# Kernel tuning notes

Measured on AMD Instinct MI355X. Metric: run time of the kernel, lower is better.

Reference implementation:

```python
import jax, jax.numpy as jnp
import numpy as np

DIM = 1024
SEQ = 4096
HEADS = 16
DH = 64
KPROJ = 64
MLP = 4096
EPS = 1e-5


def layer_norm(x, g, b):
    mu = jnp.mean(x, axis=-1, keepdims=True)
    var = jnp.mean(jnp.square(x - mu), axis=-1, keepdims=True)
    return (x - mu) * jax.lax.rsqrt(var + EPS) * g + b


def setup_inputs() -> dict:
    key = jax.random.key(0)
    ks = jax.random.split(key, 12)
    s = 0.02
    return {
        "x": jax.random.normal(ks[0], (4, SEQ, DIM), jnp.float32),
        "Wq": jax.random.normal(ks[1], (DIM, HEADS * DH), jnp.float32) * s,
        "Wk": jax.random.normal(ks[2], (DIM, HEADS * DH), jnp.float32) * s,
        "Wv": jax.random.normal(ks[3], (DIM, HEADS * DH), jnp.float32) * s,
        "E": jax.random.normal(ks[4], (SEQ, KPROJ), jnp.float32),
        "Fm": jax.random.normal(ks[5], (SEQ, KPROJ), jnp.float32),
        "Wo": jax.random.normal(ks[6], (HEADS * DH, DIM), jnp.float32) * s,
        "bo": jnp.zeros((DIM,), jnp.float32),
        "ln1_g": jnp.ones((DIM,), jnp.float32),
        "ln1_b": jnp.zeros((DIM,), jnp.float32),
        "ln2_g": jnp.ones((DIM,), jnp.float32),
        "ln2_b": jnp.zeros((DIM,), jnp.float32),
        "W1": jax.random.normal(ks[7], (DIM, MLP), jnp.float32) * s,
        "b1": jnp.zeros((MLP,), jnp.float32),
        "W2": jax.random.normal(ks[8], (MLP, DIM), jnp.float32) * s,
        "b2": jnp.zeros((DIM,), jnp.float32),
    }


def reference(x, Wq, Wk, Wv, E, Fm, Wo, bo, ln1_g, ln1_b, ln2_g, ln2_b, W1, b1, W2, b2):
    B, S, D = x.shape
    scale = DH ** -0.5
    # --- Linformer attention (pre-norm) ---
    xn = layer_norm(x, ln1_g, ln1_b)
    q = (xn @ Wq).reshape(B, S, HEADS, DH).transpose(0, 2, 1, 3)  # b h s d
    k = (xn @ Wk).reshape(B, S, HEADS, DH).transpose(0, 2, 1, 3)
    v = (xn @ Wv).reshape(B, S, HEADS, DH).transpose(0, 2, 1, 3)
    # Faithful to source: i and n are summed independently (rank-1 projection)
    kE = jnp.einsum('bhid,nk->bhkd', k, E)   # b h k d
    vF = jnp.einsum('bhid,nk->bhkd', v, Fm)  # b h k d
    dots = jnp.einsum('bhsd,bhkd->bhsk', q, kE) * scale
    attn = jax.nn.softmax(dots, axis=-1)
    out = jnp.einsum('bhsk,bhkd->bhsd', attn, vF)
    out = out.transpose(0, 2, 1, 3).reshape(B, S, HEADS * DH)
    x = x + out @ Wo + bo
    # --- MLP (pre-norm) ---
    xn2 = layer_norm(x, ln2_g, ln2_b)
    h = jax.nn.gelu(xn2 @ W1 + b1, approximate=False)
    x = x + h @ W2 + b2
    return x
```

## Files before the change

kernel.cpp:

```cpp
#include <hip/hip_runtime.h>
#include <hip/hip_bf16.h>

#define DIMD 1024
#define SEQL 4096
#define BATCH 4
#define NHEADS 16
#define DHEAD 64
#define KPROJ 64
#define MLPD 4096
#define NTOK (BATCH*SEQL)
#define EPSV 1e-5f
#define TPB 4

using short8 = __attribute__((ext_vector_type(8))) short;
using f32x4  = __attribute__((ext_vector_type(4))) float;

__device__ __forceinline__ float wave_reduce_sum(float v) {
    #pragma unroll
    for (int off = 32; off > 0; off >>= 1) v += __shfl_down(v, off, 64);
    return v;
}

__device__ __forceinline__ void async_cp16(const unsigned short* g, unsigned short* l) {
    __builtin_amdgcn_global_load_lds(
        (const __attribute__((address_space(1))) unsigned int*)g,
        (__attribute__((address_space(3))) unsigned int*)l,
        16, 0, 0);
}

__global__ __launch_bounds__(256) void k_stats1(const float* __restrict__ x,
                                                float* __restrict__ stats) {
    int t = blockIdx.x;
    const float4 x4 = *(const float4*)(x + (size_t)t*DIMD + threadIdx.x*4);
    float s  = x4.x + x4.y + x4.z + x4.w;
    float ss = x4.x*x4.x + x4.y*x4.y + x4.z*x4.z + x4.w*x4.w;
    s = wave_reduce_sum(s); ss = wave_reduce_sum(ss);
    __shared__ float rs[4], rss[4];
    int wave = threadIdx.x >> 6, lane = threadIdx.x & 63;
    if (lane == 0) { rs[wave] = s; rss[wave] = ss; }
    __syncthreads();
    if (threadIdx.x == 0) {
        float S1 = rs[0]+rs[1]+rs[2]+rs[3];
        float S2 = rss[0]+rss[1]+rss[2]+rss[3];
        float mu = S1 * (1.0f/DIMD);
        float var = S2 * (1.0f/DIMD) - mu*mu;
        stats[2*t]   = mu;
        stats[2*t+1] = rsqrtf(var + EPSV);
    }
}

__global__ __launch_bounds__(256) void k_xnsum(const float* __restrict__ x,
                                               const float* __restrict__ stats,
                                               const float* __restrict__ g1,
                                               const float* __restrict__ be1,
                                               float* __restrict__ xnsum) {
    int b = blockIdx.x >> 7, sc = blockIdx.x & 127;
    int d = threadIdx.x * 4;
    int t0 = b*SEQL + sc*32;
    float a0=0,a1=0,a2=0,a3=0;
    for (int s = 0; s < 32; s++) {
        int t = t0 + s;
        float mu = stats[2*t], rstd = stats[2*t+1];
        const float4 x4 = *(const float4*)(x + (size_t)t*DIMD + d);
        a0 += (x4.x-mu)*rstd; a1 += (x4.y-mu)*rstd;
        a2 += (x4.z-mu)*rstd; a3 += (x4.w-mu)*rstd;
    }
    const float4 g4 = *(const float4*)(g1 + d);
    const float4 b4 = *(const float4*)(be1 + d);
    atomicAdd(&xnsum[b*DIMD + d + 0], a0*g4.x + 32.0f*b4.x);
    atomicAdd(&xnsum[b*DIMD + d + 1], a1*g4.y + 32.0f*b4.y);
    atomicAdd(&xnsum[b*DIMD + d + 2], a2*g4.z + 32.0f*b4.z);
    atomicAdd(&xnsum[b*DIMD + d + 3], a3*g4.w + 32.0f*b4.w);
}

__global__ __launch_bounds__(256) void k_efsum(const float* __restrict__ E,
                                               const float* __restrict__ Fm,
                                               float* __restrict__ Esum,
                                               float* __restrict__ Fsum) {
    int g = blockIdx.x;
    int k = threadIdx.x & 63, seg = threadIdx.x >> 6;
    __shared__ float red[4][64];
    int n0 = g*256 + seg*64;
    float pe = 0, pf = 0;
    for (int i = 0; i < 64; i++) {
        pe += E [(size_t)(n0+i)*KPROJ + k];
        pf += Fm[(size_t)(n0+i)*KPROJ + k];
    }
    red[seg][k] = pe; __syncthreads();
    if (seg == 0) atomicAdd(&Esum[k], red[0][k]+red[1][k]+red[2][k]+red[3][k]);
    __syncthreads();
    red[seg][k] = pf; __syncthreads();
    if (seg == 0) atomicAdd(&Fsum[k], red[0][k]+red[1][k]+red[2][k]+red[3][k]);
}

__global__ __launch_bounds__(256) void k_kvsum(const float* __restrict__ xnsum,
                                               const float* __restrict__ Wk,
                                               const float* __restrict__ Wv,
                                               float* __restrict__ Ksum,
                                               float* __restrict__ Vsum) {
    int i = blockIdx.x;
    int dc = i & 3, jc = (i >> 2) & 3, which = (i >> 4) & 1, b = i >> 5;
    const float* W = which ? Wv : Wk;
    float* outp = which ? Vsum : Ksum;
    int j = jc*256 + threadIdx.x;
    __shared__ float xs[256];
    xs[threadIdx.x] = xnsum[b*DIMD + dc*256 + threadIdx.x];
    __syncthreads();
    float acc = 0;
    #pragma unroll 8
    for (int dd = 0; dd < 256; dd++)
        acc += xs[dd] * W[(size_t)(dc*256 + dd)*DIMD + j];
    atomicAdd(&outp[b*DIMD + j], acc);
}

__global__ __launch_bounds__(256) void k_mt(const float* __restrict__ Wq,
                                            const float* __restrict__ Ksum,
                                            float* __restrict__ Mt) {
    int i = blockIdx.x;
    int dc = i & 3, h = (i >> 2) & 15, b = i >> 6;
    __shared__ float ks[DHEAD];
    if (threadIdx.x < DHEAD) ks[threadIdx.x] = Ksum[b*DIMD + h*DHEAD + threadIdx.x];
    __syncthreads();
    int d = dc*256 + threadIdx.x;
    float acc = 0;
    #pragma unroll 8
    for (int j = 0; j < DHEAD; j++) acc += Wq[(size_t)d*DIMD + h*DHEAD + j] * ks[j];
    Mt[((size_t)b*NHEADS + h)*DIMD + d] = acc;
}

__global__ __launch_bounds__(256) void k_p(const float* __restrict__ Wo,
                                           const float* __restrict__ Vsum,
                                           float* __restrict__ P) {
    int i = blockIdx.x;
    int dc = i & 3, h = (i >> 2) & 15, b = i >> 6;
    __shared__ float vs[DHEAD];
    if (threadIdx.x < DHEAD) vs[threadIdx.x] = Vsum[b*DIMD + h*DHEAD + threadIdx.x];
    __syncthreads();
    int d = dc*256 + threadIdx.x;
    float acc = 0;
    #pragma unroll 8
    for (int j = 0; j < DHEAD; j++) acc += vs[j] * Wo[(size_t)(h*DHEAD + j)*DIMD + d];
    P[((size_t)b*NHEADS + h)*DIMD + d] = acc;
}

__global__ __launch_bounds__(256) void k_attn_apply(
    const float* __restrict__ x, const float* __restrict__ stats,
    const float* __restrict__ Mt, const float* __restrict__ P,
    const float* __restrict__ Esum, const float* __restrict__ Fsum,
    const float* __restrict__ g1, const float* __restrict__ be1,
    const float* __restrict__ bo,
    const float* __restrict__ g2, const float* __restrict__ be2,
    float* __restrict__ y, __hip_bfloat16* __restrict__ xn2) {
    __shared__ float red[TPB][NHEADS][4];
    __shared__ float w_s[TPB][NHEADS];
    __shared__ float red2[TPB][8];
    __shared__ float st2[TPB][2];
    const int t0 = blockIdx.x * TPB;
    const int b = t0 >> 12;
    const int tid = threadIdx.x;
    const int wave = tid >> 6, lane = tid & 63;
    const int d4 = tid * 4;

    const float4 g14 = *(const float4*)(g1 + d4);
    const float4 b14 = *(const float4*)(be1 + d4);
    float4 xf[TPB], xn[TPB];
    #pragma unroll
    for (int t = 0; t < TPB; t++) {
        xf[t] = *(const float4*)(x + (size_t)(t0+t)*DIMD + d4);
        float mu = stats[2*(t0+t)], rstd = stats[2*(t0+t)+1];
        xn[t].x = (xf[t].x-mu)*rstd*g14.x + b14.x;
        xn[t].y = (xf[t].y-mu)*rstd*g14.y + b14.y;
        xn[t].z = (xf[t].z-mu)*rstd*g14.z + b14.z;
        xn[t].w = (xf[t].w-mu)*rstd*g14.w + b14.w;
    }
    #pragma unroll
    for (int h = 0; h < NHEADS; h++) {
        const float4 m4 = *(const float4*)(Mt + ((size_t)b*NHEADS + h)*DIMD + d4);
        #pragma unroll
        for (int t = 0; t < TPB; t++) {
            float p = xn[t].x*m4.x + xn[t].y*m4.y + xn[t].z*m4.z + xn[t].w*m4.w;
            p = wave_reduce_sum(p);
            if (lane == 0) red[t][h][wave] = p;
        }
    }
    __syncthreads();
    {
        const float scale = 0.125f;
        const float ek = Esum[lane], fk = Fsum[lane];
        for (int pi = wave; pi < TPB*NHEADS; pi += 4) {
            int t = pi >> 4, h = pi & 15;
            float qk = red[t][h][0]+red[t][h][1]+red[t][h][2]+red[t][h][3];
            float logit = qk * scale * ek;
            float m = logit;
            #pragma unroll
            for (int off = 32; off > 0; off >>= 1) m = fmaxf(m, __shfl_down(m, off, 64));
            m = __shfl(m, 0, 64);
            float e = expf(logit - m);
            float s1 = e, s2 = e * fk;
            #pragma unroll
            for (int off = 32; off > 0; off >>= 1) {
                s1 += __shfl_down(s1, off, 64);
                s2 += __shfl_down(s2, off, 64);
            }
            if (lane == 0) w_s[t][h] = s2 / s1;
        }
    }
    __syncthreads();
    const float4 bo4 = *(const float4*)(bo + d4);
    #pragma unroll
    for (int t = 0; t < TPB; t++) {
        xf[t].x += bo4.x; xf[t].y += bo4.y; xf[t].z += bo4.z; xf[t].w += bo4.w;
    }
    #pragma unroll
    for (int h = 0; h < NHEADS; h++) {
        const float4 p4 = *(const float4*)(P + ((size_t)b*NHEADS + h)*DIMD + d4);
        #pragma unroll
        for (int t = 0; t < TPB; t++) {
            float wv = w_s[t][h];
            xf[t].x += wv*p4.x; xf[t].y += wv*p4.y;
            xf[t].z += wv*p4.z; xf[t].w += wv*p4.w;
        }
    }
    #pragma unroll
    for (int t = 0; t < TPB; t++) {
        *(float4*)(y + (size_t)(t0+t)*DIMD + d4) = xf[t];
        float s  = xf[t].x+xf[t].y+xf[t].z+xf[t].w;
        float ss = xf[t].x*xf[t].x+xf[t].y*xf[t].y+xf[t].z*xf[t].z+xf[t].w*xf[t].w;
        s = wave_reduce_sum(s); ss = wave_reduce_sum(ss);
        if (lane == 0) { red2[t][wave] = s; red2[t][4+wave] = ss; }
    }
    __syncthreads();
    if (tid < TPB) {
        float S1 = red2[tid][0]+red2[tid][1]+red2[tid][2]+red2[tid][3];
        float S2 = red2[tid][4]+red2[tid][5]+red2[tid][6]+red2[tid][7];
        float m2 = S1*(1.0f/DIMD);
        float v2 = S2*(1.0f/DIMD) - m2*m2;
        st2[tid][0] = m2; st2[tid][1] = rsqrtf(v2 + EPSV);
    }
    __syncthreads();
    const float4 g24 = *(const float4*)(g2 + d4);
    const float4 b24 = *(const float4*)(be2 + d4);
    #pragma unroll
    for (int t = 0; t < TPB; t++) {
        float mu2 = st2[t][0], rs2 = st2[t][1];
        union { __hip_bfloat16 h4[4]; uint2 v; } pk;
        pk.h4[0] = __float2bfloat16((xf[t].x-mu2)*rs2*g24.x + b24.x);
        pk.h4[1] = __float2bfloat16((xf[t].y-mu2)*rs2*g24.y + b24.y);
        pk.h4[2] = __float2bfloat16((xf[t].z-mu2)*rs2*g24.z + b24.z);
        pk.h4[3] = __float2bfloat16((xf[t].w-mu2)*rs2*g24.w + b24.w);
        *(uint2*)((char*)(xn2 + (size_t)(t0+t)*DIMD + d4)) = pk.v;
    }
}

__global__ __launch_bounds__(256) void k_transpose_bf16(const float* __restrict__ src,
                                                        __hip_bfloat16* __restrict__ dst,
                                                        int R, int C) {
    __shared__ float tile[32][33];
    int c0 = blockIdx.x * 32, r0 = blockIdx.y * 32;
    int tx = threadIdx.x & 31, ty = threadIdx.x >> 5;
    #pragma unroll
    for (int i = 0; i < 32; i += 8)
        tile[ty+i][tx] = src[(size_t)(r0+ty+i)*C + c0 + tx];
    __syncthreads();
    #pragma unroll
    for (int i = 0; i < 32; i += 8)
        dst[(size_t)(c0+ty+i)*R + r0 + tx] = __float2bfloat16(tile[tx][ty+i]);
}

template <int EPI>
__global__ __launch_bounds__(512, 2) void k_gemm256(
    const __hip_bfloat16* __restrict__ A, const __hip_bfloat16* __restrict__ Bt,
    const float* __restrict__ bias, void* __restrict__ Cout,
    int M, int N, int K) {
    __shared__ __align__(16) unsigned short As[4][8192];
    __shared__ __align__(16) unsigned short Bs[4][8192];

    const int nbx = M >> 8;
    const int m0 = (blockIdx.x % nbx) << 8;
    const int n0 = (blockIdx.x / nbx) << 8;

    const int tid  = threadIdx.x;
    const int wave = tid >> 6, lane = tid & 63;
    const int wm = (wave >> 2) * 128;
    const int wn = (wave & 3) * 64;
    const int quad = lane >> 4, l15 = lane & 15;

    f32x4 acc[8][4];
    #pragma unroll
    for (int i = 0; i < 8; i++)
        #pragma unroll
        for (int j = 0; j < 4; j++) acc[i][j] = 0;

    const int srow = tid >> 2;
    const int sq   = (tid & 3) ^ ((tid >> 3) & 3);
    const unsigned short* Au = (const unsigned short*)A;
    const unsigned short* Bu = (const unsigned short*)Bt;
    const unsigned short* Ag = Au + (size_t)(m0 + srow)*K + sq*8;
    const unsigned short* Bg = Bu + (size_t)(n0 + srow)*K + sq*8;
    const size_t halfK = 128*(size_t)K;
    unsigned short* Adst = &As[0][0] + wave*512;
    unsigned short* Bdst = &Bs[0][0] + wave*512;

    const int nk = K >> 5;
    #pragma unroll
    for (int t = 0; t < 3; t++) {
        async_cp16(Ag + t*32, Adst + t*8192);
        async_cp16(Ag + t*32 + halfK, Adst + t*8192 + 4096);
        async_cp16(Bg + t*32, Bdst + t*8192);
        async_cp16(Bg + t*32 + halfK, Bdst + t*8192 + 4096);
    }

    const int aq   = quad ^ ((l15 >> 1) & 3);
    const int aoff = (wm + l15)*32 + aq*8;
    const int boff = (wn + l15)*32 + aq*8;

    for (int j = 0; j < nk; j++) {
        __builtin_amdgcn_sched_barrier(0);
        if (j + 2 < nk)      asm volatile("s_waitcnt vmcnt(8)");
        else if (j + 1 < nk) asm volatile("s_waitcnt vmcnt(4)");
        else                 asm volatile("s_waitcnt vmcnt(0)");
        __builtin_amdgcn_sched_barrier(0);
        __builtin_amdgcn_s_barrier();
        __builtin_amdgcn_sched_barrier(0);
        if (j + 3 < nk) {
            const int t = j + 3, bb = t & 3;
            async_cp16(Ag + t*32,         &As[bb][0] + wave*512);
            async_cp16(Ag + t*32 + halfK, &As[bb][0] + wave*512 + 4096);
            async_cp16(Bg + t*32,         &Bs[bb][0] + wave*512);
            async_cp16(Bg + t*32 + halfK, &Bs[bb][0] + wave*512 + 4096);
        }
        const int b = j & 3;
        short8 af[8], bf[4];
        #pragma unroll
        for (int nf = 0; nf < 4; nf++)
            bf[nf] = *(const short8*)&Bs[b][boff + nf*512];
        #pragma unroll
        for (int mf = 0; mf < 4; mf++)
            af[mf] = *(const short8*)&As[b][aoff + mf*512];
        __builtin_amdgcn_s_setprio(1);
        #pragma unroll
        for (int mf = 0; mf < 4; mf++)
            #pragma unroll
            for (int nf = 0; nf < 4; nf++)
                acc[mf][nf] = __builtin_amdgcn_mfma_f32_16x16x32_bf16(af[mf], bf[nf], acc[mf][nf], 0, 0, 0);
        __builtin_amdgcn_s_setprio(0);
        #pragma unroll
        for (int mf = 4; mf < 8; mf++)
            af[mf] = *(const short8*)&As[b][aoff + mf*512];
        __builtin_amdgcn_s_setprio(1);
        #pragma unroll
        for (int mf = 4; mf < 8; mf++)
            #pragma unroll
            for (int nf = 0; nf < 4; nf++)
                acc[mf][nf] = __builtin_amdgcn_mfma_f32_16x16x32_bf16(af[mf], bf[nf], acc[mf][nf], 0, 0, 0);
        __builtin_amdgcn_s_setprio(0);
    }

    #pragma unroll
    for (int nf = 0; nf < 4; nf++) {
        const int col = n0 + wn + nf*16 + l15;
        const float bv = bias[col];
        #pragma unroll
        for (int mf = 0; mf < 8; mf++) {
            #pragma unroll
            for (int r = 0; r < 4; r++) {
                const int row = m0 + wm + mf*16 + quad*4 + r;
                float v = acc[mf][nf][r] + bv;
                if (EPI == 0) {
                    float u = 0.7978845608f * (v + 0.044715f * v * v * v);
                    float e = __expf(2.0f * u);
                    float th = 1.0f - 2.0f / (e + 1.0f);
                    float gl = 0.5f * v * (1.0f + th);
                    ((__hip_bfloat16*)Cout)[(size_t)row*N + col] = __float2bfloat16(gl);
                } else {
                    ((float*)Cout)[(size_t)row*N + col] += v;
                }
            }
        }
    }
}

extern "C" void kernel_launch(void* const* d_in, const int* in_sizes, int n_in,
                              void* d_out, int out_size, void* d_ws, size_t ws_size,
                              hipStream_t stream) {
    const float* x   = (const float*)d_in[0];
    const float* Wq  = (const float*)d_in[1];
    const float* Wk  = (const float*)d_in[2];
    const float* Wv  = (const float*)d_in[3];
    const float* E   = (const float*)d_in[4];
    const float* Fm  = (const float*)d_in[5];
    const float* Wo  = (const float*)d_in[6];
    const float* bo  = (const float*)d_in[7];
    const float* g1  = (const float*)d_in[8];
    const float* be1 = (const float*)d_in[9];
    const float* g2  = (const float*)d_in[10];
    const float* be2 = (const float*)d_in[11];
    const float* W1  = (const float*)d_in[12];
    const float* bb1 = (const float*)d_in[13];
    const float* W2  = (const float*)d_in[14];
    const float* bb2 = (const float*)d_in[15];
    float* outp = (float*)d_out;

    char* ws = (char*)d_ws;
    size_t o = 0;
    auto alloc = [&](size_t bytes) -> char* {
        char* r = ws + o;
        o = (o + bytes + 255) & ~(size_t)255;
        return r;
    };
    float* xnsum = (float*)alloc((size_t)BATCH*DIMD*4);
    float* Esum  = (float*)alloc(KPROJ*4);
    float* Fsum  = (float*)alloc(KPROJ*4);
    float* stats = (float*)alloc((size_t)NTOK*2*4);
    float* Ksum  = (float*)alloc((size_t)BATCH*DIMD*4);
    float* Vsum  = (float*)alloc((size_t)BATCH*DIMD*4);
    float* Mt    = (float*)alloc((size_t)BATCH*NHEADS*DIMD*4);
    float* P     = (float*)alloc((size_t)BATCH*NHEADS*DIMD*4);
    __hip_bfloat16* xn2  = (__hip_bfloat16*)alloc((size_t)NTOK*DIMD*2);
    __hip_bfloat16* W1T  = (__hip_bfloat16*)alloc((size_t)DIMD*MLPD*2);
    __hip_bfloat16* W2T  = (__hip_bfloat16*)alloc((size_t)MLPD*DIMD*2);
    __hip_bfloat16* hbuf = (__hip_bfloat16*)alloc((size_t)NTOK*MLPD*2);

    hipMemsetAsync(xnsum, 0, (size_t)BATCH*DIMD*4, stream);
    hipMemsetAsync(Esum, 0, KPROJ*4, stream);
    hipMemsetAsync(Fsum, 0, KPROJ*4, stream);
    hipMemsetAsync(Ksum, 0, (size_t)BATCH*DIMD*4, stream);
    hipMemsetAsync(Vsum, 0, (size_t)BATCH*DIMD*4, stream);

    k_stats1<<<dim3(NTOK), dim3(256), 0, stream>>>(x, stats);
    k_xnsum<<<dim3(BATCH*128), dim3(256), 0, stream>>>(x, stats, g1, be1, xnsum);
    k_efsum<<<dim3(16), dim3(256), 0, stream>>>(E, Fm, Esum, Fsum);
    k_kvsum<<<dim3(128), dim3(256), 0, stream>>>(xnsum, Wk, Wv, Ksum, Vsum);
    k_mt<<<dim3(256), dim3(256), 0, stream>>>(Wq, Ksum, Mt);
    k_p<<<dim3(256), dim3(256), 0, stream>>>(Wo, Vsum, P);
    k_attn_apply<<<dim3(NTOK/TPB), dim3(256), 0, stream>>>(
        x, stats, Mt, P, Esum, Fsum, g1, be1, bo, g2, be2, outp, xn2);
    k_transpose_bf16<<<dim3(MLPD/32, DIMD/32), dim3(256), 0, stream>>>(W1, W1T, DIMD, MLPD);
    k_transpose_bf16<<<dim3(DIMD/32, MLPD/32), dim3(256), 0, stream>>>(W2, W2T, MLPD, DIMD);
    k_gemm256<0><<<dim3((NTOK/256)*(MLPD/256)), dim3(512), 0, stream>>>(
        xn2, W1T, bb1, (void*)hbuf, NTOK, MLPD, DIMD);
    k_gemm256<1><<<dim3((NTOK/256)*(DIMD/256)), dim3(512), 0, stream>>>(
        hbuf, W2T, bb2, (void*)outp, NTOK, DIMD, MLPD);
}
```

Baseline: 856.6 us.

## Restructure 256x256 GEMM mainloop into 8-phase ping-pong with BK=64 double buffering

Replaces the 4-stage BK=32 LDS ring in the big GEMM kernel with a 2-buffer BK=64 layout and an 8-phase schedule. Each phase issues part of the next tile's global-to-LDS async loads, reads A and B fragments, then runs a quarter of the MFMAs between barriers. A new XOR swizzle is used for the 64-wide rows. The goal is to interleave loads and MFMAs more finely and cut barrier and waitcnt stalls, at the cost of more barriers per K step and more complex wait accounting.

```diff
diff --git a/kernel.cpp b/kernel.cpp
--- a/kernel.cpp
+++ b/kernel.cpp
@@ -272,18 +272,18 @@
     const __hip_bfloat16* __restrict__ A, const __hip_bfloat16* __restrict__ Bt,
     const float* __restrict__ bias, void* __restrict__ Cout,
     int M, int N, int K) {
-    __shared__ __align__(16) unsigned short As[4][8192];
-    __shared__ __align__(16) unsigned short Bs[4][8192];
+    __shared__ __align__(16) unsigned short As[2][256*64];
+    __shared__ __align__(16) unsigned short Bs[2][256*64];
 
     const int nbx = M >> 8;
     const int m0 = (blockIdx.x % nbx) << 8;
     const int n0 = (blockIdx.x / nbx) << 8;
 
     const int tid  = threadIdx.x;
-    const int wave = tid >> 6, lane = tid & 63;
-    const int wm = (wave >> 2) * 128;
-    const int wn = (wave & 3) * 64;
-    const int quad = lane >> 4, l15 = lane & 15;
+    const int w    = tid >> 6, l = tid & 63;
+    const int wm   = (w >> 2) * 128;
+    const int wn   = (w & 3) * 64;
+    const int quad = l >> 4, l15 = l & 15;
 
     f32x4 acc[8][4];
     #pragma unroll
@@ -291,69 +291,110 @@
         #pragma unroll
         for (int j = 0; j < 4; j++) acc[i][j] = 0;
 
-    const int srow = tid >> 2;
-    const int sq   = (tid & 3) ^ ((tid >> 3) & 3);
+    const int lr = l >> 3;
+    const int lc = ((l & 7) ^ lr) * 8;
     const unsigned short* Au = (const unsigned short*)A;
     const unsigned short* Bu = (const unsigned short*)Bt;
-    const unsigned short* Ag = Au + (size_t)(m0 + srow)*K + sq*8;
-    const unsigned short* Bg = Bu + (size_t)(n0 + srow)*K + sq*8;
-    const size_t halfK = 128*(size_t)K;
-    unsigned short* Adst = &As[0][0] + wave*512;
-    unsigned short* Bdst = &Bs[0][0] + wave*512;
-
-    const int nk = K >> 5;
-    #pragma unroll
-    for (int t = 0; t < 3; t++) {
-        async_cp16(Ag + t*32, Adst + t*8192);
-        async_cp16(Ag + t*32 + halfK, Adst + t*8192 + 4096);
-        async_cp16(Bg + t*32, Bdst + t*8192);
-        async_cp16(Bg + t*32 + halfK, Bdst + t*8192 + 4096);
-    }
-
-    const int aq   = quad ^ ((l15 >> 1) & 3);
-    const int aoff = (wm + l15)*32 + aq*8;
-    const int boff = (wn + l15)*32 + aq*8;
-
-    for (int j = 0; j < nk; j++) {
-        __builtin_amdgcn_sched_barrier(0);
-        if (j + 2 < nk)      asm volatile("s_waitcnt vmcnt(8)");
-        else if (j + 1 < nk) asm volatile("s_waitcnt vmcnt(4)");
-        else                 asm volatile("s_waitcnt vmcnt(0)");
-        __builtin_amdgcn_sched_barrier(0);
-        __builtin_amdgcn_s_barrier();
-        __builtin_amdgcn_sched_barrier(0);
-        if (j + 3 < nk) {
-            const int t = j + 3, bb = t & 3;
-            async_cp16(Ag + t*32,         &As[bb][0] + wave*512);
-            async_cp16(Ag + t*32 + halfK, &As[bb][0] + wave*512 + 4096);
-            async_cp16(Bg + t*32,         &Bs[bb][0] + wave*512);
-            async_cp16(Bg + t*32 + halfK, &Bs[bb][0] + wave*512 + 4096);
-        }
-        const int b = j & 3;
-        short8 af[8], bf[4];
-        #pragma unroll
-        for (int nf = 0; nf < 4; nf++)
-            bf[nf] = *(const short8*)&Bs[b][boff + nf*512];
-        #pragma unroll
-        for (int mf = 0; mf < 4; mf++)
-            af[mf] = *(const short8*)&As[b][aoff + mf*512];
-        __builtin_amdgcn_s_setprio(1);
-        #pragma unroll
-        for (int mf = 0; mf < 4; mf++)
-            #pragma unroll
-            for (int nf = 0; nf < 4; nf++)
-                acc[mf][nf] = __builtin_amdgcn_mfma_f32_16x16x32_bf16(af[mf], bf[nf], acc[mf][nf], 0, 0, 0);
-        __builtin_amdgcn_s_setprio(0);
-        #pragma unroll
-        for (int mf = 4; mf < 8; mf++)
-            af[mf] = *(const short8*)&As[b][aoff + mf*512];
-        __builtin_amdgcn_s_setprio(1);
-        #pragma unroll
-        for (int mf = 4; mf < 8; mf++)
-            #pragma unroll
-            for (int nf = 0; nf < 4; nf++)
-                acc[mf][nf] = __builtin_amdgcn_mfma_f32_16x16x32_bf16(af[mf], bf[nf], acc[mf][nf], 0, 0, 0);
-        __builtin_amdgcn_s_setprio(0);
+    const unsigned short* Asrc = Au + (size_t)(m0 + w*16 + lr)*K + lc;
+    const unsigned short* Bsrc = Bu + (size_t)(n0 + w*16 + lr)*K + lc;
+
+#define STAGE_A(d, h, kt) do { \
+    async_cp16(Asrc + (size_t)((h)*128)*K     + (kt)*64, &As[d][((h)*128 + w*16)*64]); \
+    async_cp16(Asrc + (size_t)((h)*128 + 8)*K + (kt)*64, &As[d][((h)*128 + w*16 + 8)*64]); \
+} while (0)
+#define STAGE_B(d, h, kt) do { \
+    async_cp16(Bsrc + (size_t)((h)*128)*K     + (kt)*64, &Bs[d][((h)*128 + w*16)*64]); \
+    async_cp16(Bsrc + (size_t)((h)*128 + 8)*K + (kt)*64, &Bs[d][((h)*128 + w*16 + 8)*64]); \
+} while (0)
+
+    const int sl0 = ((quad)     ^ (l15 & 7)) * 8;
+    const int sl1 = ((4 + quad) ^ (l15 & 7)) * 8;
+    const int arow = (wm + l15) * 64;
+    const int brow = (wn + l15) * 64;
+
+    short8 af[8], bf0[4], bf1[4];
+
+#define RD_AF(d, s) do { \
+    _Pragma("unroll") \
+    for (int mf = 0; mf < 4; mf++) { \
+        af[mf*2+0] = *(const short8*)&As[d][arow + ((s)*4+mf)*1024 + sl0]; \
+        af[mf*2+1] = *(const short8*)&As[d][arow + ((s)*4+mf)*1024 + sl1]; \
+    } } while (0)
+#define RD_BF(dst, d, s) do { \
+    _Pragma("unroll") \
+    for (int nf = 0; nf < 2; nf++) { \
+        dst[nf*2+0] = *(const short8*)&Bs[d][brow + ((s)*2+nf)*1024 + sl0]; \
+        dst[nf*2+1] = *(const short8*)&Bs[d][brow + ((s)*2+nf)*1024 + sl1]; \
+    } } while (0)
+
+#define QPH(MB, NB, BF) do { \
+    _Pragma("unroll") \
+    for (int mf = 0; mf < 4; mf++) { \
+        _Pragma("unroll") \
+        for (int nf = 0; nf < 2; nf++) { \
+            acc[(MB)+mf][(NB)+nf] = __builtin_amdgcn_mfma_f32_16x16x32_bf16(af[mf*2+0], BF[nf*2+0], acc[(MB)+mf][(NB)+nf], 0, 0, 0); \
+            acc[(MB)+mf][(NB)+nf] = __builtin_amdgcn_mfma_f32_16x16x32_bf16(af[mf*2+1], BF[nf*2+1], acc[(MB)+mf][(NB)+nf], 0, 0, 0); \
+        } \
+    } } while (0)
+
+#define PH_TAIL(MB, NB, BF) do { \
+    __builtin_amdgcn_sched_barrier(0); \
+    __builtin_amdgcn_s_barrier(); \
+    asm volatile("s_waitcnt lgkmcnt(0)" ::: "memory"); \
+    __builtin_amdgcn_sched_barrier(0); \
+    __builtin_amdgcn_s_setprio(1); \
+    QPH(MB, NB, BF); \
+    __builtin_amdgcn_s_setprio(0); \
+    __builtin_amdgcn_sched_barrier(0); \
+    __builtin_amdgcn_s_barrier(); \
+} while (0)
+
+    const int nit = K >> 7;
+
+    STAGE_B(0, 0, 0); STAGE_B(0, 1, 0); STAGE_A(0, 0, 0); STAGE_A(0, 1, 0);
+    STAGE_B(1, 0, 1); STAGE_B(1, 1, 1);
+    __builtin_amdgcn_sched_barrier(0);
+    asm volatile("s_waitcnt vmcnt(4)" ::: "memory");
+    __builtin_amdgcn_sched_barrier(0);
+    __builtin_amdgcn_s_barrier();
+
+    for (int it = 0; it < nit; ++it) {
+        const int kt0 = it*2, kt1 = it*2 + 1;
+        const bool more = (it + 1 < nit);
+        RD_AF(0, 0); RD_BF(bf0, 0, 0);
+        STAGE_A(1, 0, kt1);
+        PH_TAIL(0, 0, bf0);
+        RD_BF(bf1, 0, 1);
+        STAGE_A(1, 1, kt1);
+        PH_TAIL(0, 2, bf1);
+        RD_AF(0, 1);
+        if (more) STAGE_B(0, 0, kt0 + 2);
+        PH_TAIL(4, 2, bf1);
+        if (more) {
+            STAGE_B(0, 1, kt0 + 2);
+            __builtin_amdgcn_sched_barrier(0);
+            asm volatile("s_waitcnt vmcnt(4)" ::: "memory");
+        } else {
+            __builtin_amdgcn_sched_barrier(0);
+            asm volatile("s_waitcnt vmcnt(0)" ::: "memory");
+        }
+        PH_TAIL(4, 0, bf0);
+        RD_AF(1, 0); RD_BF(bf0, 1, 0);
+        if (more) STAGE_A(0, 0, kt0 + 2);
+        PH_TAIL(0, 0, bf0);
+        RD_BF(bf1, 1, 1);
+        if (more) STAGE_A(0, 1, kt0 + 2);
+        PH_TAIL(0, 2, bf1);
+        RD_AF(1, 1);
+        if (more) STAGE_B(1, 0, kt1 + 2);
+        PH_TAIL(4, 2, bf1);
+        if (more) {
+            STAGE_B(1, 1, kt1 + 2);
+            __builtin_amdgcn_sched_barrier(0);
+            asm volatile("s_waitcnt vmcnt(4)" ::: "memory");
+            __builtin_amdgcn_sched_barrier(0);
+        }
+        PH_TAIL(4, 0, bf0);
     }
 
     #pragma unroll
@@ -378,6 +419,12 @@
             }
         }
     }
+#undef STAGE_A
+#undef STAGE_B
+#undef RD_AF
+#undef RD_BF
+#undef QPH
+#undef PH_TAIL
 }
 
 extern "C" void kernel_launch(void* const* d_in, const int* in_sizes, int n_in,
```

New measurement: 783.3 us. 1.09x faster.
